# Performance work log

Hardware: AMD Instinct MI355X
Metric: run time of the kernel (lower is better)

Reference implementation:

```python
import jax, jax.numpy as jnp
import numpy as np

EPS = 1e-12  # layer_norm_eps

def gelu_bert(x):
    return 0.5 * x * (1.0 + jax.lax.erf(x / jnp.sqrt(2.0).astype(x.dtype)))

def sym_normalize(A):
    # D^{-1/2} A D^{-1/2} via outer-product scaling (algebraic form of diag matmuls)
    d = A.sum(-1)                      # [B,N] row sums
    dinv = jnp.power(d, -0.5)
    return A * dinv[..., :, None] * dinv[..., None, :]

def layernorm(x, g, b):
    mu = x.mean(-1, keepdims=True)
    var = ((x - mu) ** 2).mean(-1, keepdims=True)
    return (x - mu) * jax.lax.rsqrt(var + EPS) * g + b

def gcn(x, adj, w1, w2):
    x = jax.nn.relu(jnp.matmul(adj, x @ w1))   # [B,N,I]
    x = jax.nn.relu(jnp.matmul(adj, x @ w2))   # [B,N,H]
    return x

def setup_inputs() -> dict:
    B, N, H, I = 8, 1024, 768, 3072
    key = jax.random.key(0)
    ks = jax.random.split(key, 20)
    s = 0.02
    inp = {
        'nodes': jax.random.normal(ks[0], (B, N, H), jnp.float32),
        'graphs': jax.random.uniform(ks[1], (B, 2, N, N), jnp.float32),
        'gcn1_w1': jax.random.normal(ks[2], (H, I), jnp.float32) * s,
        'gcn1_w2': jax.random.normal(ks[3], (I, H), jnp.float32) * s,
        'gcn2_w1': jax.random.normal(ks[4], (H, I), jnp.float32) * s,
        'gcn2_w2': jax.random.normal(ks[5], (I, H), jnp.float32) * s,
        'exp1_w': jax.random.normal(ks[6], (H, I), jnp.float32) * s,
        'exp1_b': jnp.zeros((I,), jnp.float32),
        'col1_w': jax.random.normal(ks[7], (I, H), jnp.float32) * s,
        'col1_b': jnp.zeros((H,), jnp.float32),
        'exp2_w': jax.random.normal(ks[8], (H, I), jnp.float32) * s,
        'exp2_b': jnp.zeros((I,), jnp.float32),
        'col2_w': jax.random.normal(ks[9], (I, H), jnp.float32) * s,
        'col2_b': jnp.zeros((H,), jnp.float32),
        'gate_w': jax.random.normal(ks[10], (4 * H, H), jnp.float32) * s,
        'gate_b': jnp.zeros((H,), jnp.float32),
        'ln1_g': jnp.ones((H,), jnp.float32),
        'ln1_b': jnp.zeros((H,), jnp.float32),
        'ln2_g': jnp.ones((H,), jnp.float32),
        'ln2_b': jnp.zeros((H,), jnp.float32),
    }
    return inp

def reference(nodes, graphs, gcn1_w1, gcn1_w2, gcn2_w1, gcn2_w2,
              exp1_w, exp1_b, col1_w, col1_b, exp2_w, exp2_b, col2_w, col2_b,
              gate_w, gate_b, ln1_g, ln1_b, ln2_g, ln2_b):
    adj1 = sym_normalize(graphs[:, 0])   # [B,N,N]
    adj2 = sym_normalize(graphs[:, 1])
    g1 = gcn(nodes, adj1, gcn1_w1, gcn1_w2)  # [B,N,H]
    g2 = gcn(nodes, adj2, gcn2_w1, gcn2_w2)
    # FFN + residual + LN (dropout = identity at eval)
    g1 = gelu_bert(g1 @ exp1_w + exp1_b) @ col1_w + col1_b
    g1 = layernorm(nodes + g1, ln1_g, ln1_b)
    g2 = gelu_bert(g2 @ exp2_w + exp2_b) @ col2_w + col2_b
    g2 = layernorm(nodes + g2, ln2_g, ln2_b)
    gate_in = jnp.concatenate((g1, g2, g1 + g2, g1 - g2), axis=2)  # [B,N,4H]
    gate = jax.nn.sigmoid(gate_in @ gate_w + gate_b)
    return gate * g1 + (1.0 - gate) * g2
```

## Files before the change

kernel.cpp:

```cpp
#include <hip/hip_runtime.h>
#include <hip/hip_bf16.h>

typedef __bf16 b8v __attribute__((ext_vector_type(8)));
typedef float  f4v __attribute__((ext_vector_type(4)));
typedef unsigned long long ull;

#define AS3(p)  ((__attribute__((address_space(3))) void*)(p))
#define AS1C(p) ((const __attribute__((address_space(1))) void*)(p))
#define MFMA16(a, b, c) __builtin_amdgcn_mfma_f32_16x16x32_bf16((a), (b), (c), 0, 0, 0)

template<int EPI>
__global__ __launch_bounds__(512, 2) void gemm256(
    const __hip_bfloat16* __restrict__ A,  long long sA,
    const __hip_bfloat16* __restrict__ Bt, long long sBg, long long sBb, int ldB,
    __hip_bfloat16* __restrict__ C, long long sC, int ldC,
    const float* __restrict__ bias0, const float* __restrict__ bias1, int K)
{
  const int bz = blockIdx.z;
  A  += (long long)bz * sA;
  Bt += (long long)(bz >> 3) * sBg + (long long)(bz & 7) * sBb;
  const float* __restrict__ bias = (bz & 1) ? bias1 : bias0;

  __shared__ __hip_bfloat16 As[2][2][8192];
  __shared__ __hip_bfloat16 Bs[2][2][8192];

  const int tid  = threadIdx.x;
  const int lane = tid & 63;
  const int wave = tid >> 6;
  const int wr = wave >> 2;
  const int wc = wave & 3;
  const int lm = lane & 15;
  const int kq = lane >> 4;

  const long long m0 = (long long)blockIdx.x * 256;
  const long long n0 = (long long)blockIdx.y * 256;

  const int sr  = tid >> 3;
  const int sc  = tid & 7;
  const int gch = sc ^ (sr & 7);
  const int ldsE = tid * 8;

  auto stageA = [&](int d, int h, int kt) {
    const __hip_bfloat16* s0 = A + (m0 + h * 128 + sr) * (long long)K + (long long)kt * 64 + gch * 8;
    __builtin_amdgcn_global_load_lds(AS1C(s0),            AS3(&As[d][h][ldsE]),        16, 0, 0);
    __builtin_amdgcn_global_load_lds(AS1C(s0 + 64LL * K), AS3(&As[d][h][4096 + ldsE]), 16, 0, 0);
  };
  auto stageB = [&](int d, int h, int kt) {
    const __hip_bfloat16* s0 = Bt + (n0 + h * 128 + sr) * (long long)ldB + (long long)kt * 64 + gch * 8;
    __builtin_amdgcn_global_load_lds(AS1C(s0),              AS3(&Bs[d][h][ldsE]),        16, 0, 0);
    __builtin_amdgcn_global_load_lds(AS1C(s0 + 64LL * ldB), AS3(&Bs[d][h][4096 + ldsE]), 16, 0, 0);
  };

  const int NT = K >> 6;
  stageA(0, 0, 0); stageA(0, 1, 0); stageB(0, 0, 0); stageB(0, 1, 0);
  stageA(1, 0, 1);
  asm volatile("s_waitcnt vmcnt(2)" ::: "memory");
  __builtin_amdgcn_s_barrier();

  f4v acc[8][4];
  const f4v fz = {0.0f, 0.0f, 0.0f, 0.0f};
#pragma unroll
  for (int i = 0; i < 8; i++)
#pragma unroll
    for (int j = 0; j < 4; j++) acc[i][j] = fz;

  const int rb  = lm * 64;
  const int cs0 = ((kq)     ^ (lm & 7)) * 8;
  const int cs1 = ((4 + kq) ^ (lm & 7)) * 8;

  for (int kt = 0; kt < NT; ++kt) {
    const int d = kt & 1, dn = d ^ 1;
    const __hip_bfloat16* Ab = &As[d][wr][0];
    const __hip_bfloat16* Bb = &Bs[d][wc >> 1][(wc & 1) * 4096];
    const bool st1 = (kt + 1 < NT);
    b8v afL[8], afH[8], bfL[4], bfH[4];

#pragma unroll
    for (int f = 0; f < 4; f++) {
      afL[f * 2]     = *(const b8v*)(Ab + f * 1024 + rb + cs0);
      afL[f * 2 + 1] = *(const b8v*)(Ab + f * 1024 + rb + cs1);
    }
#pragma unroll
    for (int f = 0; f < 2; f++) {
      bfL[f * 2]     = *(const b8v*)(Bb + f * 1024 + rb + cs0);
      bfL[f * 2 + 1] = *(const b8v*)(Bb + f * 1024 + rb + cs1);
    }
    if (st1) stageA(dn, 1, kt + 1);
    __builtin_amdgcn_s_barrier();
    asm volatile("s_waitcnt lgkmcnt(0)" ::: "memory");
    __builtin_amdgcn_sched_barrier(0);
    __builtin_amdgcn_s_setprio(1);
#pragma unroll
    for (int i = 0; i < 4; i++)
#pragma unroll
      for (int j = 0; j < 2; j++) acc[i][j] = MFMA16(bfL[j * 2], afL[i * 2], acc[i][j]);
#pragma unroll
    for (int i = 0; i < 4; i++)
#pragma unroll
      for (int j = 0; j < 2; j++) acc[i][j] = MFMA16(bfL[j * 2 + 1], afL[i * 2 + 1], acc[i][j]);
    __builtin_amdgcn_s_setprio(0);
    __builtin_amdgcn_s_barrier();

#pragma unroll
    for (int f = 0; f < 2; f++) {
      bfH[f * 2]     = *(const b8v*)(Bb + (2 + f) * 1024 + rb + cs0);
      bfH[f * 2 + 1] = *(const b8v*)(Bb + (2 + f) * 1024 + rb + cs1);
    }
    if (st1) stageB(dn, 0, kt + 1);
    __builtin_amdgcn_s_barrier();
    asm volatile("s_waitcnt lgkmcnt(0)" ::: "memory");
    __builtin_amdgcn_sched_barrier(0);
    __builtin_amdgcn_s_setprio(1);
#pragma unroll
    for (int i = 0; i < 4; i++)
#pragma unroll
      for (int j = 0; j < 2; j++) acc[i][2 + j] = MFMA16(bfH[j * 2], afL[i * 2], acc[i][2 + j]);
#pragma unroll
    for (int i = 0; i < 4; i++)
#pragma unroll
      for (int j = 0; j < 2; j++) acc[i][2 + j] = MFMA16(bfH[j * 2 + 1], afL[i * 2 + 1], acc[i][2 + j]);
    __builtin_amdgcn_s_setprio(0);
    __builtin_amdgcn_s_barrier();

#pragma unroll
    for (int f = 0; f < 4; f++) {
      afH[f * 2]     = *(const b8v*)(Ab + (4 + f) * 1024 + rb + cs0);
      afH[f * 2 + 1] = *(const b8v*)(Ab + (4 + f) * 1024 + rb + cs1);
    }
    if (st1) stageB(dn, 1, kt + 1);
    __builtin_amdgcn_s_barrier();
    asm volatile("s_waitcnt lgkmcnt(0)" ::: "memory");
    __builtin_amdgcn_sched_barrier(0);
    __builtin_amdgcn_s_setprio(1);
#pragma unroll
    for (int i = 0; i < 4; i++)
#pragma unroll
      for (int j = 0; j < 2; j++) acc[4 + i][j] = MFMA16(bfL[j * 2], afH[i * 2], acc[4 + i][j]);
#pragma unroll
    for (int i = 0; i < 4; i++)
#pragma unroll
      for (int j = 0; j < 2; j++) acc[4 + i][j] = MFMA16(bfL[j * 2 + 1], afH[i * 2 + 1], acc[4 + i][j]);
    __builtin_amdgcn_s_setprio(0);
    __builtin_amdgcn_s_barrier();

    if (kt + 2 < NT) stageA(d, 0, kt + 2);
    __builtin_amdgcn_s_setprio(1);
#pragma unroll
    for (int i = 0; i < 4; i++)
#pragma unroll
      for (int j = 0; j < 2; j++) acc[4 + i][2 + j] = MFMA16(bfH[j * 2], afH[i * 2], acc[4 + i][2 + j]);
#pragma unroll
    for (int i = 0; i < 4; i++)
#pragma unroll
      for (int j = 0; j < 2; j++) acc[4 + i][2 + j] = MFMA16(bfH[j * 2 + 1], afH[i * 2 + 1], acc[4 + i][2 + j]);
    __builtin_amdgcn_s_setprio(0);
    if (kt + 2 < NT) asm volatile("s_waitcnt vmcnt(2)" ::: "memory");
    else             asm volatile("s_waitcnt vmcnt(0)" ::: "memory");
    __builtin_amdgcn_s_barrier();
  }

#pragma unroll
  for (int i = 0; i < 8; i++) {
    const long long row = m0 + wr * 128 + i * 16 + lm;
#pragma unroll
    for (int j = 0; j < 4; j++) {
      const int colb = (int)n0 + wc * 64 + j * 16 + kq * 4;
      float v[4];
#pragma unroll
      for (int rg = 0; rg < 4; rg++) v[rg] = acc[i][j][rg];
      if constexpr (EPI == 1) {
#pragma unroll
        for (int rg = 0; rg < 4; rg++) v[rg] = fmaxf(v[rg], 0.0f);
      }
      if constexpr (EPI == 2) {
        const float4 b4 = *(const float4*)(bias + colb);
        const float* bb = (const float*)&b4;
#pragma unroll
        for (int rg = 0; rg < 4; rg++) {
          float x = v[rg] + bb[rg];
          v[rg] = 0.5f * x * (1.0f + erff(x * 0.70710678118654752f));
        }
      }
      union { __hip_bfloat16 h[4]; ull u; } P;
#pragma unroll
      for (int rg = 0; rg < 4; rg++) P.h[rg] = __float2bfloat16(v[rg]);
      *(ull*)(C + (long long)bz * sC + row * (long long)ldC + colb) = P.u;
    }
  }
}

template<int EPI, int OBF, int ORIENT, int MP>
__global__ __launch_bounds__(256) void gemm_bt(
    const __hip_bfloat16* __restrict__ A,  long long sA,
    const __hip_bfloat16* __restrict__ Bt, long long sBg, long long sBb, int ldB,
    void* __restrict__ Cv, long long sC, int ldC,
    const float* __restrict__ bias0, const float* __restrict__ bias1,
    const __hip_bfloat16* __restrict__ gcat, int K)
{
  const int bz = blockIdx.z;
  A  += (long long)bz * sA;
  Bt += (long long)(bz >> 3) * sBg + (long long)(bz & 7) * sBb;
  const float* __restrict__ bias = (bz & 1) ? bias1 : bias0;

  __shared__ __hip_bfloat16 As[128 * 32];
  __shared__ __hip_bfloat16 Bs[128 * 32];

  const int tid  = threadIdx.x;
  const int lane = tid & 63;
  const int wave = tid >> 6;

  const long long mBase = (long long)blockIdx.x * (MP * 128);
  const long long n0    = (long long)blockIdx.y * 128;

  const int r  = tid >> 2;
  const int kc = (tid & 3) ^ ((r >> 2) & 3);
  const __hip_bfloat16* aRow = A  + (mBase + r) * (long long)K   + kc * 8;
  const __hip_bfloat16* bRow = Bt + (n0 + r)    * (long long)ldB + kc * 8;

  const int wm = (wave & 1) * 64;
  const int wn = (wave >> 1) * 64;
  const int lm = lane & 15;
  const int kq = lane >> 4;

  const int sw   = (lm >> 2) & 3;
  const int aOff = (wm + lm) * 32 + (kq ^ sw) * 8;
  const int bOff = (wn + lm) * 32 + (kq ^ sw) * 8;

  auto stage = [&](long long aoff, int k0) {
    const __hip_bfloat16* a = aRow + aoff + k0;
    const __hip_bfloat16* b = bRow + k0;
    __builtin_amdgcn_global_load_lds(AS1C(a),              AS3(As + tid * 8),        16, 0, 0);
    __builtin_amdgcn_global_load_lds(AS1C(a + 64LL * K),   AS3(As + 2048 + tid * 8), 16, 0, 0);
    __builtin_amdgcn_global_load_lds(AS1C(b),              AS3(Bs + tid * 8),        16, 0, 0);
    __builtin_amdgcn_global_load_lds(AS1C(b + 64LL * ldB), AS3(Bs + 2048 + tid * 8), 16, 0, 0);
  };

  stage(0, 0);

  const f4v fzero = {0.0f, 0.0f, 0.0f, 0.0f};
  char* Cb = (char*)Cv;

  for (int p = 0; p < MP; ++p) {
    const long long aoff = (long long)p * 128 * K;

    f4v acc[4][4];
#pragma unroll
    for (int i = 0; i < 4; i++)
#pragma unroll
      for (int j = 0; j < 4; j++) acc[i][j] = fzero;

    for (int k0 = 0; k0 < K; k0 += 32) {
      __syncthreads();

      b8v af[4], bf[4];
#pragma unroll
      for (int i = 0; i < 4; i++) af[i] = *(const b8v*)(As + aOff + i * 16 * 32);
#pragma unroll
      for (int j = 0; j < 4; j++) bf[j] = *(const b8v*)(Bs + bOff + j * 16 * 32);

      __syncthreads();

      if (k0 + 32 < K)            stage(aoff, k0 + 32);
      else if (MP > 1 && p + 1 < MP) stage(aoff + 128LL * K, 0);

#pragma unroll
      for (int i = 0; i < 4; i++)
#pragma unroll
        for (int j = 0; j < 4; j++) {
          if constexpr (ORIENT == 0)
            acc[i][j] = __builtin_amdgcn_mfma_f32_16x16x32_bf16(bf[j], af[i], acc[i][j], 0, 0, 0);
          else
            acc[i][j] = __builtin_amdgcn_mfma_f32_16x16x32_bf16(af[i], bf[j], acc[i][j], 0, 0, 0);
        }
    }

    const long long m0 = mBase + (long long)p * 128;
#pragma unroll
    for (int i = 0; i < 4; i++) {
#pragma unroll
      for (int j = 0; j < 4; j++) {
        float v[4];
#pragma unroll
        for (int rg = 0; rg < 4; rg++) v[rg] = acc[i][j][rg];

        if constexpr (ORIENT == 0) {
          const long long row  = m0 + wm + i * 16 + lm;
          const int       colb = (int)n0 + wn + j * 16 + kq * 4;
          if constexpr (EPI == 1) {
#pragma unroll
            for (int rg = 0; rg < 4; rg++) v[rg] = fmaxf(v[rg], 0.0f);
          }
          if constexpr (EPI == 2) {
            const float4 b4 = *(const float4*)(bias + colb);
            const float* bb = (const float*)&b4;
#pragma unroll
            for (int rg = 0; rg < 4; rg++) {
              float x = v[rg] + bb[rg];
              v[rg] = 0.5f * x * (1.0f + erff(x * 0.70710678118654752f));
            }
          }
          const long long base = bz * sC + row * (long long)ldC + colb;
          if constexpr (EPI == 3) {
            const float4 b4 = *(const float4*)(bias0 + colb);
            const float* bb = (const float*)&b4;
            union { __hip_bfloat16 h[4]; ull u; } g1, g2;
            g1.u = *(const ull*)(gcat + row * 1536 + colb);
            g2.u = *(const ull*)(gcat + row * 1536 + 768 + colb);
            float o[4];
#pragma unroll
            for (int rg = 0; rg < 4; rg++) {
              const float s = 1.0f / (1.0f + expf(-(v[rg] + bb[rg])));
              o[rg] = s * __bfloat162float(g1.h[rg]) +
                      (1.0f - s) * __bfloat162float(g2.h[rg]);
            }
            *(float4*)(Cb + base * 4) = *(const float4*)o;
          } else if constexpr (OBF) {
            union { __hip_bfloat16 h[4]; ull u; } P;
#pragma unroll
            for (int rg = 0; rg < 4; rg++) P.h[rg] = __float2bfloat16(v[rg]);
            *(ull*)(Cb + base * 2) = P.u;
          } else {
            *(float4*)(Cb + base * 4) = *(const float4*)v;
          }
        } else {
          const long long crow = n0 + wn + j * 16 + lm;
          const long long mb   = m0 + wm + i * 16 + kq * 4;
          if constexpr (EPI == 1) {
#pragma unroll
            for (int rg = 0; rg < 4; rg++) v[rg] = fmaxf(v[rg], 0.0f);
          }
          const long long base = bz * sC + crow * (long long)ldC + mb;
          if constexpr (OBF) {
            union { __hip_bfloat16 h[4]; ull u; } P;
#pragma unroll
            for (int rg = 0; rg < 4; rg++) P.h[rg] = __float2bfloat16(v[rg]);
            *(ull*)(Cb + base * 2) = P.u;
          } else {
            *(float4*)(Cb + base * 4) = *(const float4*)v;
          }
        }
      }
    }
  }
}

__global__ __launch_bounds__(256) void rowsum_dinv(const float* __restrict__ g,
                                                   float* __restrict__ dinv)
{
  const int wave = threadIdx.x >> 6, lane = threadIdx.x & 63;
  const long long row = (long long)blockIdx.x * 4 + wave;
  const float4* p = (const float4*)(g + row * 1024);
  float s = 0.0f;
#pragma unroll
  for (int k = 0; k < 4; k++) {
    float4 v = p[lane + k * 64];
    s += v.x + v.y + v.z + v.w;
  }
#pragma unroll
  for (int o = 32; o > 0; o >>= 1) s += __shfl_down(s, o);
  if (lane == 0) dinv[row] = 1.0f / sqrtf(s);
}

__global__ __launch_bounds__(256) void scale_adj(const float* __restrict__ g,
                                                 const float* __restrict__ dinv,
                                                 __hip_bfloat16* __restrict__ out)
{
  const long long t = (long long)blockIdx.x * 256 + threadIdx.x;
  const long long e = t * 4;
  const int m = (int)(e >> 20);
  const int i = (int)((e >> 10) & 1023);
  const int j = (int)(e & 1023);
  const float4 v  = *(const float4*)(g + e);
  const float  di = dinv[m * 1024 + i];
  const float4 dj = *(const float4*)(dinv + m * 1024 + j);
  const int om = (m & 1) * 8 + (m >> 1);
  union { __hip_bfloat16 h[4]; ull u; } r;
  r.h[0] = __float2bfloat16(v.x * di * dj.x);
  r.h[1] = __float2bfloat16(v.y * di * dj.y);
  r.h[2] = __float2bfloat16(v.z * di * dj.z);
  r.h[3] = __float2bfloat16(v.w * di * dj.w);
  *(ull*)(out + ((long long)om << 20) + (long long)i * 1024 + j) = r.u;
}

template<typename TIN>
__global__ void transpose_conv(const TIN* __restrict__ in, __hip_bfloat16* __restrict__ out,
                               int R, int C, long long sIn, long long sOut)
{
  __shared__ __hip_bfloat16 tile[32][33];
  in  += (long long)blockIdx.z * sIn;
  out += (long long)blockIdx.z * sOut;
  const int c0 = blockIdx.x * 32, r0 = blockIdx.y * 32;
  const int tx = threadIdx.x, ty = threadIdx.y;
#pragma unroll
  for (int i = 0; i < 32; i += 8)
    tile[ty + i][tx] = __float2bfloat16((float)in[(long long)(r0 + ty + i) * C + c0 + tx]);
  __syncthreads();
#pragma unroll
  for (int i = 0; i < 32; i += 8)
    out[(long long)(c0 + ty + i) * R + r0 + tx] = tile[tx][ty + i];
}

__global__ __launch_bounds__(256) void ln_residual2(
    const float* __restrict__ nodes, const __hip_bfloat16* __restrict__ V,
    const float* __restrict__ colb0, const float* __restrict__ colb1,
    const float* __restrict__ lng0,  const float* __restrict__ lng1,
    const float* __restrict__ lnb0,  const float* __restrict__ lnb1,
    __hip_bfloat16* __restrict__ gcat)
{
  const long long row = blockIdx.x;
  const int g = (int)(row >> 13);
  const long long rr = row & 8191;
  const float* __restrict__ colb = g ? colb1 : colb0;
  const float* __restrict__ lng  = g ? lng1  : lng0;
  const float* __restrict__ lnb  = g ? lnb1  : lnb0;
  const int t = threadIdx.x;
  const long long nbase = rr * 768;
  const long long vbase = row * 768;
  float x[3]; float s = 0.0f, ss = 0.0f;
#pragma unroll
  for (int i = 0; i < 3; i++) {
    const int c = t + i * 256;
    const float v = nodes[nbase + c] + __bfloat162float(V[vbase + c]) + colb[c];
    x[i] = v; s += v; ss += v * v;
  }
  __shared__ float red[8];
#pragma unroll
  for (int o = 32; o > 0; o >>= 1) { s += __shfl_down(s, o); ss += __shfl_down(ss, o); }
  const int wave = t >> 6, lane = t & 63;
  if (lane == 0) { red[wave] = s; red[4 + wave] = ss; }
  __syncthreads();
  if (t == 0) {
    red[0] = red[0] + red[1] + red[2] + red[3];
    red[4] = red[4] + red[5] + red[6] + red[7];
  }
  __syncthreads();
  const float mu  = red[0] * (1.0f / 768.0f);
  float var = red[4] * (1.0f / 768.0f) - mu * mu;
  var = fmaxf(var, 0.0f);
  const float rs = rsqrtf(var + 1e-12f);
#pragma unroll
  for (int i = 0; i < 3; i++) {
    const int c = t + i * 256;
    const float y = (x[i] - mu) * rs * lng[c] + lnb[c];
    gcat[rr * 1536 + g * 768 + c] = __float2bfloat16(y);
  }
}

__global__ __launch_bounds__(256) void build_wefft(const float* __restrict__ gw,
                                                   __hip_bfloat16* __restrict__ wt)
{
  const int idx = blockIdx.x * 256 + threadIdx.x;
  const int n = idx / 1536, k = idx % 1536;
  float v;
  if (k < 768) v = gw[k * 768 + n] + gw[(1536 + k) * 768 + n] + gw[(2304 + k) * 768 + n];
  else {
    const int kk = k - 768;
    v = gw[(768 + kk) * 768 + n] + gw[(1536 + kk) * 768 + n] - gw[(2304 + kk) * 768 + n];
  }
  wt[idx] = __float2bfloat16(v);
}

extern "C" void kernel_launch(void* const* d_in, const int* in_sizes, int n_in,
                              void* d_out, int out_size, void* d_ws, size_t ws_size,
                              hipStream_t stream)
{
  const float* nodes  = (const float*)d_in[0];
  const float* graphs = (const float*)d_in[1];
  const float* gcn_w1[2] = { (const float*)d_in[2], (const float*)d_in[4] };
  const float* gcn_w2[2] = { (const float*)d_in[3], (const float*)d_in[5] };
  const float* exp_w[2]  = { (const float*)d_in[6],  (const float*)d_in[10] };
  const float* exp_b[2]  = { (const float*)d_in[7],  (const float*)d_in[11] };
  const float* col_w[2]  = { (const float*)d_in[8],  (const float*)d_in[12] };
  const float* col_b[2]  = { (const float*)d_in[9],  (const float*)d_in[13] };
  const float* gate_w = (const float*)d_in[14];
  const float* gate_b = (const float*)d_in[15];
  const float* ln_g[2] = { (const float*)d_in[16], (const float*)d_in[18] };
  const float* ln_b[2] = { (const float*)d_in[17], (const float*)d_in[19] };
  float* out = (float*)d_out;

  char* w = (char*)d_ws;
  auto alloc = [&](size_t bytes) { char* p = w; w += (bytes + 255) & ~(size_t)255; return p; };
  float*          dinv   = (float*)alloc(16384ULL * 4);
  char*           regA   = alloc(16ULL * 1024 * 1024 * 2);
  __hip_bfloat16* adj2   = (__hip_bfloat16*)regA;
  __hip_bfloat16* Gcat   = (__hip_bfloat16*)regA;
  __hip_bfloat16* wefft  = (__hip_bfloat16*)alloc(768ULL * 1536 * 2);
  __hip_bfloat16* bufA2  = (__hip_bfloat16*)alloc(16ULL * 1024 * 768 * 2);
  char*           regD   = alloc(16ULL * 1024 * 768 * 2);
  __hip_bfloat16* Xt     = (__hip_bfloat16*)regD;
  __hip_bfloat16* bufB2  = (__hip_bfloat16*)regD;
  __hip_bfloat16* X12    = (__hip_bfloat16*)alloc(2ULL * 8192 * 3072 * 2);
  __hip_bfloat16* wgt1   = (__hip_bfloat16*)alloc(2ULL * 3072 * 768 * 2);
  __hip_bfloat16* wgt2   = (__hip_bfloat16*)alloc(2ULL * 768 * 3072 * 2);

  const long long sW1 = 3072LL * 768;
  const long long sW2 = 768LL * 3072;
  const long long sNM = 1024LL * 768;
  const long long sBig = 8192LL * 3072;

  rowsum_dinv<<<4096, 256, 0, stream>>>(graphs, dinv);
  transpose_conv<float><<<dim3(24, 32, 8), dim3(32, 8), 0, stream>>>(
      nodes, Xt, 1024, 768, 1024LL * 768, 768LL * 1024);
  build_wefft<<<4608, 256, 0, stream>>>(gate_w, wefft);
  scale_adj<<<16384, 256, 0, stream>>>(graphs, dinv, adj2);
  for (int g = 0; g < 2; g++) {
    transpose_conv<float><<<dim3(96, 24, 1), dim3(32, 8), 0, stream>>>(
        gcn_w1[g], wgt1 + g * sW1, 768, 3072, 0, 0);
    transpose_conv<float><<<dim3(24, 96, 1), dim3(32, 8), 0, stream>>>(
        gcn_w2[g], wgt2 + g * sW2, 3072, 768, 0, 0);
  }

  gemm256<0><<<dim3(4, 3, 16), 512, 0, stream>>>(
      adj2, 1LL << 20, Xt, 0, sNM, 1024, bufA2, sNM, 768,
      nullptr, nullptr, 1024);
  gemm256<1><<<dim3(32, 12, 2), 512, 0, stream>>>(
      bufA2, 8192LL * 768, wgt1, 0, sW1, 768, X12, sBig, 3072,
      nullptr, nullptr, 768);
  gemm256<0><<<dim3(3, 32, 2), 512, 0, stream>>>(
      wgt2, sW2, X12, 0, sBig, 3072, bufA2, 768LL * 8192, 8192,
      nullptr, nullptr, 3072);
  for (int g = 0; g < 2; g++) {
    transpose_conv<float><<<dim3(96, 24, 1), dim3(32, 8), 0, stream>>>(
        exp_w[g], wgt1 + g * sW1, 768, 3072, 0, 0);
    transpose_conv<float><<<dim3(24, 96, 1), dim3(32, 8), 0, stream>>>(
        col_w[g], wgt2 + g * sW2, 3072, 768, 0, 0);
  }
  gemm256<1><<<dim3(4, 3, 16), 512, 0, stream>>>(
      adj2, 1LL << 20, bufA2, 768LL * 8192, 1024, 8192, bufB2, sNM, 768,
      nullptr, nullptr, 1024);
  gemm256<2><<<dim3(32, 12, 2), 512, 0, stream>>>(
      bufB2, 8192LL * 768, wgt1, 0, sW1, 768, X12, sBig, 3072,
      exp_b[0], exp_b[1], 768);
  gemm256<0><<<dim3(32, 3, 2), 512, 0, stream>>>(
      X12, sBig, wgt2, 0, sW2, 3072, bufA2, 8192LL * 768, 768,
      nullptr, nullptr, 3072);
  ln_residual2<<<16384, 256, 0, stream>>>(
      nodes, bufA2, col_b[0], col_b[1], ln_g[0], ln_g[1], ln_b[0], ln_b[1], Gcat);
  gemm_bt<3, 0, 0, 1><<<dim3(64, 6, 1), 256, 0, stream>>>(
      Gcat, 0, wefft, 0, 0, 1536, out, 0, 768,
      gate_b, nullptr, Gcat, 1536);
}
```

Before: 803.8 us.

## Restructure GEMM k-loop staging to prefetch next-tile B fragments early

Reorganizes the 256x256 bf16 MFMA GEMM main loop. Each staging call now loads a full A or B tile (four global-to-LDS loads) instead of the split half-tiles with the two-ahead A prefetch. The first B fragments of the next k-tile are read from LDS during the last compute phase of the current iteration, with vmcnt waits placed to match. The aim is to hide LDS read latency at the start of each iteration and to simplify the prefetch schedule. In exchange, less global prefetch depth is kept in flight, and the extra barriers and changed waitcnt accounting could expose memory latency or introduce hazards.

New measurement: 833.9 us. +3.7%, slower.

```diff
diff --git a/kernel.cpp b/kernel.cpp
--- a/kernel.cpp
+++ b/kernel.cpp
@@ -40,22 +40,22 @@
   const int gch = sc ^ (sr & 7);
   const int ldsE = tid * 8;
 
-  auto stageA = [&](int d, int h, int kt) {
-    const __hip_bfloat16* s0 = A + (m0 + h * 128 + sr) * (long long)K + (long long)kt * 64 + gch * 8;
-    __builtin_amdgcn_global_load_lds(AS1C(s0),            AS3(&As[d][h][ldsE]),        16, 0, 0);
-    __builtin_amdgcn_global_load_lds(AS1C(s0 + 64LL * K), AS3(&As[d][h][4096 + ldsE]), 16, 0, 0);
+  auto stageA = [&](int d, int kt) {
+    const __hip_bfloat16* s0 = A + (m0 + sr) * (long long)K + (long long)kt * 64 + gch * 8;
+    __builtin_amdgcn_global_load_lds(AS1C(s0),              AS3(&As[d][0][ldsE]),        16, 0, 0);
+    __builtin_amdgcn_global_load_lds(AS1C(s0 + 64LL * K),   AS3(&As[d][0][4096 + ldsE]), 16, 0, 0);
+    __builtin_amdgcn_global_load_lds(AS1C(s0 + 128LL * K),  AS3(&As[d][1][ldsE]),        16, 0, 0);
+    __builtin_amdgcn_global_load_lds(AS1C(s0 + 192LL * K),  AS3(&As[d][1][4096 + ldsE]), 16, 0, 0);
   };
-  auto stageB = [&](int d, int h, int kt) {
-    const __hip_bfloat16* s0 = Bt + (n0 + h * 128 + sr) * (long long)ldB + (long long)kt * 64 + gch * 8;
-    __builtin_amdgcn_global_load_lds(AS1C(s0),              AS3(&Bs[d][h][ldsE]),        16, 0, 0);
-    __builtin_amdgcn_global_load_lds(AS1C(s0 + 64LL * ldB), AS3(&Bs[d][h][4096 + ldsE]), 16, 0, 0);
+  auto stageB = [&](int d, int kt) {
+    const __hip_bfloat16* s0 = Bt + (n0 + sr) * (long long)ldB + (long long)kt * 64 + gch * 8;
+    __builtin_amdgcn_global_load_lds(AS1C(s0),               AS3(&Bs[d][0][ldsE]),        16, 0, 0);
+    __builtin_amdgcn_global_load_lds(AS1C(s0 + 64LL * ldB),  AS3(&Bs[d][0][4096 + ldsE]), 16, 0, 0);
+    __builtin_amdgcn_global_load_lds(AS1C(s0 + 128LL * ldB), AS3(&Bs[d][1][ldsE]),        16, 0, 0);
+    __builtin_amdgcn_global_load_lds(AS1C(s0 + 192LL * ldB), AS3(&Bs[d][1][4096 + ldsE]), 16, 0, 0);
   };
 
   const int NT = K >> 6;
-  stageA(0, 0, 0); stageA(0, 1, 0); stageB(0, 0, 0); stageB(0, 1, 0);
-  stageA(1, 0, 1);
-  asm volatile("s_waitcnt vmcnt(2)" ::: "memory");
-  __builtin_amdgcn_s_barrier();
 
   f4v acc[8][4];
   const f4v fz = {0.0f, 0.0f, 0.0f, 0.0f};
@@ -68,24 +68,35 @@
   const int cs0 = ((kq)     ^ (lm & 7)) * 8;
   const int cs1 = ((4 + kq) ^ (lm & 7)) * 8;
 
+  stageA(0, 0); stageB(0, 0);
+  asm volatile("s_waitcnt vmcnt(2)" ::: "memory");
+  __builtin_amdgcn_s_barrier();
+
+  b8v bfL[4];
+  {
+    const __hip_bfloat16* Bb0 = &Bs[0][wc >> 1][(wc & 1) * 4096];
+#pragma unroll
+    for (int f = 0; f < 2; f++) {
+      bfL[f * 2]     = *(const b8v*)(Bb0 + f * 1024 + rb + cs0);
+      bfL[f * 2 + 1] = *(const b8v*)(Bb0 + f * 1024 + rb + cs1);
+    }
+  }
+
   for (int kt = 0; kt < NT; ++kt) {
     const int d = kt & 1, dn = d ^ 1;
-    const __hip_bfloat16* Ab = &As[d][wr][0];
-    const __hip_bfloat16* Bb = &Bs[d][wc >> 1][(wc & 1) * 4096];
+    const __hip_bfloat16* Ab  = &As[d][wr][0];
+    const __hip_bfloat16* Bb  = &Bs[d][wc >> 1][(wc & 1) * 4096];
+    const __hip_bfloat16* Bbn = &Bs[dn][wc >> 1][(wc & 1) * 4096];
     const bool st1 = (kt + 1 < NT);
-    b8v afL[8], afH[8], bfL[4], bfH[4];
-
+    b8v afL[8], afH[8], bfH[4];
+
+    __builtin_amdgcn_s_barrier();
 #pragma unroll
     for (int f = 0; f < 4; f++) {
       afL[f * 2]     = *(const b8v*)(Ab + f * 1024 + rb + cs0);
       afL[f * 2 + 1] = *(const b8v*)(Ab + f * 1024 + rb + cs1);
     }
-#pragma unroll
-    for (int f = 0; f < 2; f++) {
-      bfL[f * 2]     = *(const b8v*)(Bb + f * 1024 + rb + cs0);
-      bfL[f * 2 + 1] = *(const b8v*)(Bb + f * 1024 + rb + cs1);
-    }
-    if (st1) stageA(dn, 1, kt + 1);
+    if (st1) stageA(dn, kt + 1);
     __builtin_amdgcn_s_barrier();
     asm volatile("s_waitcnt lgkmcnt(0)" ::: "memory");
     __builtin_amdgcn_sched_barrier(0);
@@ -99,14 +110,16 @@
 #pragma unroll
       for (int j = 0; j < 2; j++) acc[i][j] = MFMA16(bfL[j * 2 + 1], afL[i * 2 + 1], acc[i][j]);
     __builtin_amdgcn_s_setprio(0);
-    __builtin_amdgcn_s_barrier();
-
+
+    if (st1) asm volatile("s_waitcnt vmcnt(4)" ::: "memory");
+    else     asm volatile("s_waitcnt vmcnt(0)" ::: "memory");
+    __builtin_amdgcn_s_barrier();
 #pragma unroll
     for (int f = 0; f < 2; f++) {
       bfH[f * 2]     = *(const b8v*)(Bb + (2 + f) * 1024 + rb + cs0);
       bfH[f * 2 + 1] = *(const b8v*)(Bb + (2 + f) * 1024 + rb + cs1);
     }
-    if (st1) stageB(dn, 0, kt + 1);
+    if (st1) stageB(dn, kt + 1);
     __builtin_amdgcn_s_barrier();
     asm volatile("s_waitcnt lgkmcnt(0)" ::: "memory");
     __builtin_amdgcn_sched_barrier(0);
@@ -120,14 +133,13 @@
 #pragma unroll
       for (int j = 0; j < 2; j++) acc[i][2 + j] = MFMA16(bfH[j * 2 + 1], afL[i * 2 + 1], acc[i][2 + j]);
     __builtin_amdgcn_s_setprio(0);
-    __builtin_amdgcn_s_barrier();
-
+
+    __builtin_amdgcn_s_barrier();
 #pragma unroll
     for (int f = 0; f < 4; f++) {
       afH[f * 2]     = *(const b8v*)(Ab + (4 + f) * 1024 + rb + cs0);
       afH[f * 2 + 1] = *(const b8v*)(Ab + (4 + f) * 1024 + rb + cs1);
     }
-    if (st1) stageB(dn, 1, kt + 1);
     __builtin_amdgcn_s_barrier();
     asm volatile("s_waitcnt lgkmcnt(0)" ::: "memory");
     __builtin_amdgcn_sched_barrier(0);
@@ -141,9 +153,19 @@
 #pragma unroll
       for (int j = 0; j < 2; j++) acc[4 + i][j] = MFMA16(bfL[j * 2 + 1], afH[i * 2 + 1], acc[4 + i][j]);
     __builtin_amdgcn_s_setprio(0);
-    __builtin_amdgcn_s_barrier();
-
-    if (kt + 2 < NT) stageA(d, 0, kt + 2);
+
+    if (st1) asm volatile("s_waitcnt vmcnt(2)" ::: "memory");
+    __builtin_amdgcn_s_barrier();
+    if (st1) {
+#pragma unroll
+      for (int f = 0; f < 2; f++) {
+        bfL[f * 2]     = *(const b8v*)(Bbn + f * 1024 + rb + cs0);
+        bfL[f * 2 + 1] = *(const b8v*)(Bbn + f * 1024 + rb + cs1);
+      }
+    }
+    __builtin_amdgcn_s_barrier();
+    asm volatile("s_waitcnt lgkmcnt(0)" ::: "memory");
+    __builtin_amdgcn_sched_barrier(0);
     __builtin_amdgcn_s_setprio(1);
 #pragma unroll
     for (int i = 0; i < 4; i++)
@@ -154,9 +176,6 @@
 #pragma unroll
       for (int j = 0; j < 2; j++) acc[4 + i][2 + j] = MFMA16(bfH[j * 2 + 1], afH[i * 2 + 1], acc[4 + i][2 + j]);
     __builtin_amdgcn_s_setprio(0);
-    if (kt + 2 < NT) asm volatile("s_waitcnt vmcnt(2)" ::: "memory");
-    else             asm volatile("s_waitcnt vmcnt(0)" ::: "memory");
-    __builtin_amdgcn_s_barrier();
   }
 
 #pragma unroll
```
